# Kernel optimization log

Hardware: AMD Instinct MI355X
Metric: run time of the kernel (lower is better)

Reference implementation:

```python
import jax, jax.numpy as jnp
import numpy as np
import math

N, E = 50000, 800000
N_BASIS, N_ATOM, L = 32, 128, 2
START, STOP = 0.0, 10.0

_idx = [(i, j, L - i - j) for i in range(L + 1) for j in range(L + 1 - i)]
IP = np.array([t[0] for t in _idx], np.float32)
JP = np.array([t[1] for t in _idx], np.float32)
KP = np.array([t[2] for t in _idx], np.float32)
_d = np.array([math.factorial(a) * math.factorial(b) * math.factorial(c) for a, b, c in _idx], np.float32)
PREF2 = np.sqrt(math.factorial(L) / _d).astype(np.float32)  # [T], T = (L+1)(L+2)/2 = 6
OFFSETS = np.linspace(START, STOP, N_BASIS, dtype=np.float32)
WIDTH = np.float32(OFFSETS[1] - OFFSETS[0])


def _signed_pow(x, p):
    # matches torch.pow for negative base with integer-valued float exponent
    p = np.asarray(p)
    odd = (p.astype(np.int64) % 2 == 1)
    r = jnp.abs(x)[:, None] ** jnp.asarray(p)[None, :]
    return jnp.where((x < 0.0)[:, None] & jnp.asarray(odd)[None, :], -r, r)


def setup_inputs() -> dict:
    key = jax.random.key(0)
    ks = jax.random.split(key, 12)
    s = 0.05
    return {
        "feat": jax.random.normal(ks[0], (N, N_ATOM), jnp.float32),
        "dis_vec": jax.random.normal(ks[1], (E, 3), jnp.float32),
        "cj_w1": jax.random.normal(ks[2], (N_ATOM, N_ATOM), jnp.float32) * s,
        "cj_b1": jnp.zeros((N_ATOM,), jnp.float32),
        "cj_w2": jax.random.normal(ks[3], (N_ATOM, 1), jnp.float32) * s,
        "cj_b2": jnp.zeros((1,), jnp.float32),
        "msg_w1": jax.random.normal(ks[4], (N_BASIS, N_ATOM), jnp.float32) * s,
        "msg_b1": jnp.zeros((N_ATOM,), jnp.float32),
        "msg_w2": jax.random.normal(ks[5], (N_ATOM, N_ATOM), jnp.float32) * s,
        "msg_b2": jnp.zeros((N_ATOM,), jnp.float32),
        "filt_w1": jax.random.normal(ks[6], (IP.shape[0], IP.shape[0]), jnp.float32) * s,
        "filt_w2": jax.random.normal(ks[7], (IP.shape[0], 1), jnp.float32) * s,
        "filt_b2": jnp.zeros((1,), jnp.float32),
        "src": jax.random.randint(ks[8], (E,), 0, N, jnp.int32),
        "dst": jax.random.randint(ks[9], (E,), 0, N, jnp.int32),
    }


def reference(feat, dis_vec, cj_w1, cj_b1, cj_w2, cj_b2, msg_w1, msg_b1, msg_w2, msg_b2, filt_w1, filt_w2, filt_b2, src, dst):
    silu = jax.nn.silu  # swish
    # polynomial prefactor: [E, T]
    phix = _signed_pow(dis_vec[:, 0] + 1e-8, IP)
    phiy = _signed_pow(dis_vec[:, 1] + 1e-8, JP)
    phiz = _signed_pow(dis_vec[:, 2] + 1e-8, KP)
    prefactor = phix * phiy * phiz
    # gaussian basis: [E, n_basis] (cutoff_network is None -> C = 1)
    dis = jnp.linalg.norm(dis_vec + 1e-9, axis=-1)
    coeff = -0.5 / (WIDTH ** 2)
    g0 = jnp.exp(coeff * (dis[:, None] - jnp.asarray(OFFSETS)[None, :]) ** 2)
    # gauss: [E, n_basis, T]
    gauss = prefactor[:, None, :] * g0[:, :, None] * jnp.asarray(PREF2)[None, None, :]
    # cj = cj_mlp(feat): [N, 1]
    cj = silu(feat @ cj_w1 + cj_b1) @ cj_w2 + cj_b2
    # e_mul_v: gather dst-node scalar onto edges; copy_e_sum(g.reverse()): scatter-sum to src nodes
    fij = gauss * cj[dst][:, :, None]  # [E, n_basis, T]
    agg = jax.ops.segment_sum(fij, src, num_segments=N)  # [N, n_basis, T]
    f2 = jnp.sum(agg ** 2, axis=-1)  # [N, n_basis]
    msg_in = f2 / (jnp.linalg.norm(f2 + 1e-9, axis=-1, keepdims=True) + 1.0)
    msg_out = silu(msg_in @ msg_w1 + msg_b1) @ msg_w2 + msg_b2  # [N, n_atom_basis]
    gn = gauss / (jnp.linalg.norm(gauss + 1e-8, axis=-1) + 1.0)[..., None]
    filt = (silu(gn @ filt_w1) @ filt_w2 + filt_b2)[..., 0]  # [E, n_basis]
    return msg_out, filt
```

## Files before the change

kernel.cpp:

```cpp
#include <hip/hip_runtime.h>
#include <math.h>

#define N_NODES 50000
#define N_EDGES 800000
#define NB 32
#define NA 128
#define CJ_BLOCKS 782
#define CNT_BLOCKS 3125
#define EDGE_BLOCKS 3125
#define SCAN_BLOCKS 49

constexpr double STEP_D = 10.0 / 31.0;
constexpr float  STEP_F = (float)(10.0 / 31.0);
constexpr float  COEFF  = -0.5f / (STEP_F * STEP_F);
constexpr float  R2     = 1.41421356237309515f;
constexpr float  INV_STEP = 3.1f;
constexpr float  HWIN   = 2.05f;

__device__ __forceinline__ float fast_rcp(float x) {
    return __builtin_amdgcn_rcpf(x);
}

__device__ __forceinline__ float silu_f(float x) {
    return x * fast_rcp(1.0f + __expf(-x));
}

__global__ __launch_bounds__(256) void k_cj_count(const float* __restrict__ feat,
                                                  const float* __restrict__ w1,
                                                  const float* __restrict__ b1,
                                                  const float* __restrict__ w2,
                                                  const float* __restrict__ b2,
                                                  float* __restrict__ cj,
                                                  const int* __restrict__ src,
                                                  int* __restrict__ cnt) {
    __shared__ float fls[64 * 128];
    int tid = threadIdx.x;
    int blk = blockIdx.x;
    if (blk >= CJ_BLOCKS) {
        int e = (blk - CJ_BLOCKS) * 256 + tid;
        if (e < N_EDGES) atomicAdd(&cnt[src[e]], 1);
        return;
    }
    int jq  = tid & 31;
    int ng  = tid >> 5;
    int j0  = jq * 4;
    int n0  = blk * 64;

    {
        const float4* fp = (const float4*)feat;
        int base = n0 * 32;
        int maxi = N_NODES * 32 - 1;
#pragma unroll
        for (int r = 0; r < 8; r++) {
            int idx = base + r * 256 + tid;
            ((float4*)fls)[r * 256 + tid] = fp[min(idx, maxi)];
        }
    }
    __syncthreads();

    float4 bv = *(const float4*)&b1[j0];
    float h[8][4];
#pragma unroll
    for (int i = 0; i < 8; i++) {
        h[i][0] = bv.x; h[i][1] = bv.y; h[i][2] = bv.z; h[i][3] = bv.w;
    }
    for (int kb = 0; kb < 128; kb += 4) {
        float4 wv[4];
#pragma unroll
        for (int u = 0; u < 4; u++) wv[u] = *(const float4*)&w1[(kb + u) * 128 + j0];
#pragma unroll
        for (int i = 0; i < 8; i++) {
            float4 f4 = *(const float4*)&fls[(ng * 8 + i) * 128 + kb];
            h[i][0] = fmaf(f4.x, wv[0].x, h[i][0]);
            h[i][1] = fmaf(f4.x, wv[0].y, h[i][1]);
            h[i][2] = fmaf(f4.x, wv[0].z, h[i][2]);
            h[i][3] = fmaf(f4.x, wv[0].w, h[i][3]);
            h[i][0] = fmaf(f4.y, wv[1].x, h[i][0]);
            h[i][1] = fmaf(f4.y, wv[1].y, h[i][1]);
            h[i][2] = fmaf(f4.y, wv[1].z, h[i][2]);
            h[i][3] = fmaf(f4.y, wv[1].w, h[i][3]);
            h[i][0] = fmaf(f4.z, wv[2].x, h[i][0]);
            h[i][1] = fmaf(f4.z, wv[2].y, h[i][1]);
            h[i][2] = fmaf(f4.z, wv[2].z, h[i][2]);
            h[i][3] = fmaf(f4.z, wv[2].w, h[i][3]);
            h[i][0] = fmaf(f4.w, wv[3].x, h[i][0]);
            h[i][1] = fmaf(f4.w, wv[3].y, h[i][1]);
            h[i][2] = fmaf(f4.w, wv[3].z, h[i][2]);
            h[i][3] = fmaf(f4.w, wv[3].w, h[i][3]);
        }
    }
    float4 w2v = *(const float4*)&w2[j0];
    float keep = 0.f;
#pragma unroll
    for (int i = 0; i < 8; i++) {
        float v = silu_f(h[i][0]) * w2v.x + silu_f(h[i][1]) * w2v.y
                + silu_f(h[i][2]) * w2v.z + silu_f(h[i][3]) * w2v.w;
#pragma unroll
        for (int m = 1; m < 32; m <<= 1) v += __shfl_xor(v, m, 64);
        if (jq == i) keep = v;
    }
    if (jq < 8) {
        int n = n0 + ng * 8 + jq;
        if (n < N_NODES) cj[n] = b2[0] + keep;
    }
}

__global__ __launch_bounds__(1024) void k_scan1(const int* __restrict__ cnt,
                                                int* __restrict__ offs,
                                                int* __restrict__ bsum) {
    __shared__ int s[1024];
    int i = blockIdx.x * 1024 + threadIdx.x;
    int v = (i < N_NODES) ? cnt[i] : 0;
    s[threadIdx.x] = v;
    __syncthreads();
    for (int o = 1; o < 1024; o <<= 1) {
        int t = (threadIdx.x >= (unsigned)o) ? s[threadIdx.x - o] : 0;
        __syncthreads();
        s[threadIdx.x] += t;
        __syncthreads();
    }
    if (i < N_NODES) offs[i] = s[threadIdx.x] - v;
    if (threadIdx.x == 1023) bsum[blockIdx.x] = s[1023];
}

__global__ __launch_bounds__(1024) void k_scan2(int* __restrict__ offs,
                                                const int* __restrict__ bsum,
                                                int* __restrict__ cursor) {
    __shared__ int sbase;
    if (threadIdx.x < 64) {
        int lane = threadIdx.x;
        int v = (lane < blockIdx.x) ? bsum[lane] : 0;
#pragma unroll
        for (int m = 1; m < 64; m <<= 1) v += __shfl_xor(v, m, 64);
        if (lane == 0) sbase = v;
    }
    __syncthreads();
    int i = blockIdx.x * 1024 + threadIdx.x;
    if (i < N_NODES) {
        int v = offs[i] + sbase;
        offs[i] = v;
        cursor[i] = v;
    }
}

__global__ __launch_bounds__(256) void k_edge(const int* __restrict__ src,
                                              const int* __restrict__ dst,
                                              const float* __restrict__ dis_vec,
                                              const float* __restrict__ cj,
                                              int* __restrict__ cursor,
                                              float* __restrict__ sedge,
                                              const float* __restrict__ fw1,
                                              const float* __restrict__ fw2,
                                              const float* __restrict__ fb2,
                                              float* __restrict__ outf) {
    __shared__ float buf[256 * 36];
    int tid = threadIdx.x;
    int e = blockIdx.x * 256 + tid;
    int se = src[e];
    int de = dst[e];
    float dx = dis_vec[3 * e], dy = dis_vec[3 * e + 1], dz = dis_vec[3 * e + 2];
    float cjd = cj[de];
    int p = atomicAdd(&cursor[se], 1);

    float ax = dx + 1e-9f, ay = dy + 1e-9f, az = dz + 1e-9f;
    float dis = sqrtf(ax * ax + ay * ay + az * az);
    float x = dx + 1e-8f, y = dy + 1e-8f, z = dz + 1e-8f;
    float pre[6];
    pre[0] = z * z;      pre[1] = y * z * R2; pre[2] = y * y;
    pre[3] = x * z * R2; pre[4] = x * y * R2; pre[5] = x * x;

    {
        float4* op = (float4*)(sedge + (size_t)p * 8);
        op[0] = make_float4(dis, pre[0] * cjd, pre[1] * cjd, pre[2] * cjd);
        op[1] = make_float4(pre[3] * cjd, pre[4] * cjd, pre[5] * cjd, 0.f);
    }

    float A = 0.f, B = 0.f;
#pragma unroll
    for (int t = 0; t < 6; t++) { A = fmaf(pre[t], pre[t], A); B += pre[t]; }
    float q[6];
#pragma unroll
    for (int tp = 0; tp < 6; tp++) {
        float s = 0.f;
#pragma unroll
        for (int t = 0; t < 6; t++) s = fmaf(pre[t], fw1[t * 6 + tp], s);
        q[tp] = s;
    }
    float bias = fb2[0];
    float w2r[6];
#pragma unroll
    for (int t = 0; t < 6; t++) w2r[t] = fw2[t];

    float* row = &buf[tid * 36];
    float4 b4v = make_float4(bias, bias, bias, bias);
#pragma unroll
    for (int r = 0; r < 8; r++) ((float4*)row)[r] = b4v;

    int b_lo = (int)ceilf((dis - HWIN) * INV_STEP);
#pragma unroll
    for (int k = 0; k < 14; k++) {
        int b = b_lo + k;
        float offb = (float)((double)b * STEP_D);
        float dd = dis - offb;
        float g = __expf(COEFF * dd * dd);
        float ns = fmaf(g * g, A, fmaf(2e-8f * g, B, 6e-16f));
        float rn = fast_rcp(sqrtf(ns) + 1.0f);
        float s = g * rn;
        float o = bias;
#pragma unroll
        for (int tp = 0; tp < 6; tp++) o = fmaf(silu_f(s * q[tp]), w2r[tp], o);
        if ((unsigned)b < 32u) row[b] = o;
    }
    __syncthreads();

    float4* ob = (float4*)(outf + (size_t)blockIdx.x * (256 * 32));
#pragma unroll
    for (int r = 0; r < 8; r++) {
        int g = r * 256 + tid;
        int eloc = g >> 3, j = g & 7;
        ob[g] = *(const float4*)&buf[eloc * 36 + j * 4];
    }
}

__global__ __launch_bounds__(256) void k_agg(const float* __restrict__ sedge,
                                             const int* __restrict__ offs,
                                             const int* __restrict__ cnt,
                                             float* __restrict__ msg_in) {
    int lane = threadIdx.x & 63;
    int n = blockIdx.x * 4 + (threadIdx.x >> 6);
    if (n >= N_NODES) return;
    int b = lane >> 1, th = lane & 1;
    float offb = (float)((double)b * STEP_D);
    int beg = offs[n];
    int deg = cnt[n];
    const float4* sp = (const float4*)sedge + (size_t)beg * 2;
    float a0 = 0.f, a1 = 0.f, a2 = 0.f;
    int i = 0;
    for (; i + 2 <= deg; i += 2) {
        float4 r0 = sp[0], r1 = sp[1], r2 = sp[2], r3 = sp[3];
        sp += 4;
        float dd0 = r0.x - offb;
        float dd1 = r2.x - offb;
        float g0 = __expf(COEFF * dd0 * dd0);
        float g1 = __expf(COEFF * dd1 * dd1);
        float w00 = th ? r1.x : r0.y, w01 = th ? r1.y : r0.z, w02 = th ? r1.z : r0.w;
        float w10 = th ? r3.x : r2.y, w11 = th ? r3.y : r2.z, w12 = th ? r3.z : r2.w;
        a0 = fmaf(g0, w00, a0);
        a1 = fmaf(g0, w01, a1);
        a2 = fmaf(g0, w02, a2);
        a0 = fmaf(g1, w10, a0);
        a1 = fmaf(g1, w11, a1);
        a2 = fmaf(g1, w12, a2);
    }
    if (i < deg) {
        float4 r0 = sp[0], r1 = sp[1];
        float dd0 = r0.x - offb;
        float g0 = __expf(COEFF * dd0 * dd0);
        float w00 = th ? r1.x : r0.y, w01 = th ? r1.y : r0.z, w02 = th ? r1.z : r0.w;
        a0 = fmaf(g0, w00, a0);
        a1 = fmaf(g0, w01, a1);
        a2 = fmaf(g0, w02, a2);
    }
    float s = a0 * a0 + a1 * a1 + a2 * a2;
    float f2 = s + __shfl_xor(s, 1, 64);
    float p = f2 + 1e-9f;
    p = p * p;
    float tot = p;
#pragma unroll
    for (int m = 1; m < 64; m <<= 1) tot += __shfl_xor(tot, m, 64);
    float nrm = sqrtf(0.5f * tot);
    float val = f2 * fast_rcp(nrm + 1.0f);
    if (th == 0) msg_in[(size_t)n * NB + b] = val;
}

__global__ __launch_bounds__(256) void k_msg(const float* __restrict__ msg_in,
                                             const float* __restrict__ w1,
                                             const float* __restrict__ b1,
                                             const float* __restrict__ w2,
                                             const float* __restrict__ b2,
                                             float* __restrict__ out) {
    __shared__ float mi[64 * 32];
    __shared__ float sh[64 * 128];
    int tid = threadIdx.x;
    int jq  = tid & 31;
    int ng  = tid >> 5;
    int j0  = jq * 4;
    int n0  = blockIdx.x * 64;

    {
        const float4* srcp = (const float4*)msg_in;
        int base = n0 * 8;
        int maxi = N_NODES * 8 - 1;
#pragma unroll
        for (int r = 0; r < 2; r++) {
            int idx = base + r * 256 + tid;
            ((float4*)mi)[r * 256 + tid] = srcp[min(idx, maxi)];
        }
    }
    __syncthreads();

    float4 b1v = *(const float4*)&b1[j0];
    float h[8][4];
#pragma unroll
    for (int i = 0; i < 8; i++) {
        h[i][0] = b1v.x; h[i][1] = b1v.y; h[i][2] = b1v.z; h[i][3] = b1v.w;
    }
#pragma unroll
    for (int bb = 0; bb < 32; bb += 4) {
        float4 wv[4];
#pragma unroll
        for (int u = 0; u < 4; u++) wv[u] = *(const float4*)&w1[(bb + u) * 128 + j0];
#pragma unroll
        for (int i = 0; i < 8; i++) {
            float4 m4 = *(const float4*)&mi[(ng * 8 + i) * 32 + bb];
            h[i][0] = fmaf(m4.x, wv[0].x, h[i][0]);
            h[i][1] = fmaf(m4.x, wv[0].y, h[i][1]);
            h[i][2] = fmaf(m4.x, wv[0].z, h[i][2]);
            h[i][3] = fmaf(m4.x, wv[0].w, h[i][3]);
            h[i][0] = fmaf(m4.y, wv[1].x, h[i][0]);
            h[i][1] = fmaf(m4.y, wv[1].y, h[i][1]);
            h[i][2] = fmaf(m4.y, wv[1].z, h[i][2]);
            h[i][3] = fmaf(m4.y, wv[1].w, h[i][3]);
            h[i][0] = fmaf(m4.z, wv[2].x, h[i][0]);
            h[i][1] = fmaf(m4.z, wv[2].y, h[i][1]);
            h[i][2] = fmaf(m4.z, wv[2].z, h[i][2]);
            h[i][3] = fmaf(m4.z, wv[2].w, h[i][3]);
            h[i][0] = fmaf(m4.w, wv[3].x, h[i][0]);
            h[i][1] = fmaf(m4.w, wv[3].y, h[i][1]);
            h[i][2] = fmaf(m4.w, wv[3].z, h[i][2]);
            h[i][3] = fmaf(m4.w, wv[3].w, h[i][3]);
        }
    }
#pragma unroll
    for (int i = 0; i < 8; i++) {
        float4 sv = make_float4(silu_f(h[i][0]), silu_f(h[i][1]),
                                silu_f(h[i][2]), silu_f(h[i][3]));
        *(float4*)&sh[(ng * 8 + i) * 128 + j0] = sv;
    }
    __syncthreads();

    float4 b2v = *(const float4*)&b2[j0];
    float acc[8][4];
#pragma unroll
    for (int i = 0; i < 8; i++) {
        acc[i][0] = b2v.x; acc[i][1] = b2v.y; acc[i][2] = b2v.z; acc[i][3] = b2v.w;
    }
    for (int hb = 0; hb < 128; hb += 4) {
        float4 wv[4];
#pragma unroll
        for (int u = 0; u < 4; u++) wv[u] = *(const float4*)&w2[(hb + u) * 128 + j0];
#pragma unroll
        for (int i = 0; i < 8; i++) {
            float4 s4 = *(const float4*)&sh[(ng * 8 + i) * 128 + hb];
            acc[i][0] = fmaf(s4.x, wv[0].x, acc[i][0]);
            acc[i][1] = fmaf(s4.x, wv[0].y, acc[i][1]);
            acc[i][2] = fmaf(s4.x, wv[0].z, acc[i][2]);
            acc[i][3] = fmaf(s4.x, wv[0].w, acc[i][3]);
            acc[i][0] = fmaf(s4.y, wv[1].x, acc[i][0]);
            acc[i][1] = fmaf(s4.y, wv[1].y, acc[i][1]);
            acc[i][2] = fmaf(s4.y, wv[1].z, acc[i][2]);
            acc[i][3] = fmaf(s4.y, wv[1].w, acc[i][3]);
            acc[i][0] = fmaf(s4.z, wv[2].x, acc[i][0]);
            acc[i][1] = fmaf(s4.z, wv[2].y, acc[i][1]);
            acc[i][2] = fmaf(s4.z, wv[2].z, acc[i][2]);
            acc[i][3] = fmaf(s4.z, wv[2].w, acc[i][3]);
            acc[i][0] = fmaf(s4.w, wv[3].x, acc[i][0]);
            acc[i][1] = fmaf(s4.w, wv[3].y, acc[i][1]);
            acc[i][2] = fmaf(s4.w, wv[3].z, acc[i][2]);
            acc[i][3] = fmaf(s4.w, wv[3].w, acc[i][3]);
        }
    }
#pragma unroll
    for (int i = 0; i < 8; i++) {
        int n = n0 + ng * 8 + i;
        if (n < N_NODES) {
            *(float4*)&out[(size_t)n * 128 + j0] =
                make_float4(acc[i][0], acc[i][1], acc[i][2], acc[i][3]);
        }
    }
}

extern "C" void kernel_launch(void* const* d_in, const int* in_sizes, int n_in,
                              void* d_out, int out_size, void* d_ws, size_t ws_size,
                              hipStream_t stream) {
    (void)in_sizes; (void)n_in; (void)out_size; (void)ws_size;
    const float* feat    = (const float*)d_in[0];
    const float* dis_vec = (const float*)d_in[1];
    const float* cj_w1   = (const float*)d_in[2];
    const float* cj_b1   = (const float*)d_in[3];
    const float* cj_w2   = (const float*)d_in[4];
    const float* cj_b2   = (const float*)d_in[5];
    const float* msg_w1  = (const float*)d_in[6];
    const float* msg_b1  = (const float*)d_in[7];
    const float* msg_w2  = (const float*)d_in[8];
    const float* msg_b2  = (const float*)d_in[9];
    const float* filt_w1 = (const float*)d_in[10];
    const float* filt_w2 = (const float*)d_in[11];
    const float* filt_b2 = (const float*)d_in[12];
    const int*   src     = (const int*)d_in[13];
    const int*   dst     = (const int*)d_in[14];
    float* out = (float*)d_out;

    float* ws     = (float*)d_ws;
    float* cj     = ws;
    float* msg_in = cj + 50048;
    int*   cnt    = (int*)(msg_in + 1600256);
    int*   offs   = cnt + 50048;
    int*   cursor = offs + 50048;
    int*   bsum   = cursor + 50048;
    int*   bbase  = bsum + 64;
    float* sedge  = (float*)(bbase + 64);

    hipMemsetAsync(cnt, 0, N_NODES * sizeof(int), stream);

    k_cj_count<<<CJ_BLOCKS + CNT_BLOCKS, 256, 0, stream>>>(feat, cj_w1, cj_b1, cj_w2,
                                                           cj_b2, cj, src, cnt);
    k_scan1<<<SCAN_BLOCKS, 1024, 0, stream>>>(cnt, offs, bsum);
    k_scan2<<<SCAN_BLOCKS, 1024, 0, stream>>>(offs, bsum, cursor);
    k_edge<<<EDGE_BLOCKS, 256, 0, stream>>>(src, dst, dis_vec, cj, cursor, sedge,
                                            filt_w1, filt_w2, filt_b2,
                                            out + (size_t)N_NODES * NA);
    k_agg<<<(N_NODES + 3) / 4, 256, 0, stream>>>(sedge, offs, cnt, msg_in);
    k_msg<<<(N_NODES + 63) / 64, 256, 0, stream>>>(msg_in, msg_w1, msg_b1, msg_w2, msg_b2, out);
}
```

Before: 350.4 us.

## Fuse scan passes with decoupled lookback and merge aggregation into message MLP

The two scan kernels become one kernel that publishes block sums through atomics and spin-waits on earlier blocks (a decoupled-lookback style prefix). The per-node aggregation kernel is folded into the message MLP kernel. Each wave aggregates 16 nodes into shared memory, which removes the msg_in round trip through global memory and two launches. The cost is fewer blocks and wave-serial per-node loops with shuffle-heavy inner work, which lowers aggregation parallelism. The spin-wait also relies on all 49 scan blocks being co-resident.

```diff
diff --git a/kernel.cpp b/kernel.cpp
--- a/kernel.cpp
+++ b/kernel.cpp
@@ -9,6 +9,7 @@
 #define CNT_BLOCKS 3125
 #define EDGE_BLOCKS 3125
 #define SCAN_BLOCKS 49
+#define AGG_BLOCKS 782
 
 constexpr double STEP_D = 10.0 / 31.0;
 constexpr float  STEP_F = (float)(10.0 / 31.0);
@@ -105,11 +106,14 @@
     }
 }
 
-__global__ __launch_bounds__(1024) void k_scan1(const int* __restrict__ cnt,
-                                                int* __restrict__ offs,
-                                                int* __restrict__ bsum) {
+__global__ __launch_bounds__(1024) void k_scan(const int* __restrict__ cnt,
+                                               int* __restrict__ offs,
+                                               int* __restrict__ cursor,
+                                               int* __restrict__ bsum) {
     __shared__ int s[1024];
-    int i = blockIdx.x * 1024 + threadIdx.x;
+    __shared__ int sbase;
+    int bid = blockIdx.x;
+    int i = bid * 1024 + threadIdx.x;
     int v = (i < N_NODES) ? cnt[i] : 0;
     s[threadIdx.x] = v;
     __syncthreads();
@@ -119,27 +123,24 @@
         s[threadIdx.x] += t;
         __syncthreads();
     }
-    if (i < N_NODES) offs[i] = s[threadIdx.x] - v;
-    if (threadIdx.x == 1023) bsum[blockIdx.x] = s[1023];
-}
-
-__global__ __launch_bounds__(1024) void k_scan2(int* __restrict__ offs,
-                                                const int* __restrict__ bsum,
-                                                int* __restrict__ cursor) {
-    __shared__ int sbase;
+    if (threadIdx.x == 1023) atomicExch(&bsum[bid], s[1023] + 1);
     if (threadIdx.x < 64) {
         int lane = threadIdx.x;
-        int v = (lane < blockIdx.x) ? bsum[lane] : 0;
-#pragma unroll
-        for (int m = 1; m < 64; m <<= 1) v += __shfl_xor(v, m, 64);
-        if (lane == 0) sbase = v;
-    }
-    __syncthreads();
-    int i = blockIdx.x * 1024 + threadIdx.x;
+        int val = 0;
+        if (lane < bid) {
+            int t;
+            do { t = atomicAdd(&bsum[lane], 0); } while (t == 0);
+            val = t - 1;
+        }
+#pragma unroll
+        for (int m = 1; m < 64; m <<= 1) val += __shfl_xor(val, m, 64);
+        if (lane == 0) sbase = val;
+    }
+    __syncthreads();
     if (i < N_NODES) {
-        int v = offs[i] + sbase;
-        offs[i] = v;
-        cursor[i] = v;
+        int o2 = s[threadIdx.x] - v + sbase;
+        offs[i] = o2;
+        cursor[i] = o2;
     }
 }
 
@@ -222,82 +223,68 @@
     }
 }
 
-__global__ __launch_bounds__(256) void k_agg(const float* __restrict__ sedge,
-                                             const int* __restrict__ offs,
-                                             const int* __restrict__ cnt,
-                                             float* __restrict__ msg_in) {
-    int lane = threadIdx.x & 63;
-    int n = blockIdx.x * 4 + (threadIdx.x >> 6);
-    if (n >= N_NODES) return;
-    int b = lane >> 1, th = lane & 1;
-    float offb = (float)((double)b * STEP_D);
-    int beg = offs[n];
-    int deg = cnt[n];
-    const float4* sp = (const float4*)sedge + (size_t)beg * 2;
-    float a0 = 0.f, a1 = 0.f, a2 = 0.f;
-    int i = 0;
-    for (; i + 2 <= deg; i += 2) {
-        float4 r0 = sp[0], r1 = sp[1], r2 = sp[2], r3 = sp[3];
-        sp += 4;
-        float dd0 = r0.x - offb;
-        float dd1 = r2.x - offb;
-        float g0 = __expf(COEFF * dd0 * dd0);
-        float g1 = __expf(COEFF * dd1 * dd1);
-        float w00 = th ? r1.x : r0.y, w01 = th ? r1.y : r0.z, w02 = th ? r1.z : r0.w;
-        float w10 = th ? r3.x : r2.y, w11 = th ? r3.y : r2.z, w12 = th ? r3.z : r2.w;
-        a0 = fmaf(g0, w00, a0);
-        a1 = fmaf(g0, w01, a1);
-        a2 = fmaf(g0, w02, a2);
-        a0 = fmaf(g1, w10, a0);
-        a1 = fmaf(g1, w11, a1);
-        a2 = fmaf(g1, w12, a2);
-    }
-    if (i < deg) {
-        float4 r0 = sp[0], r1 = sp[1];
-        float dd0 = r0.x - offb;
-        float g0 = __expf(COEFF * dd0 * dd0);
-        float w00 = th ? r1.x : r0.y, w01 = th ? r1.y : r0.z, w02 = th ? r1.z : r0.w;
-        a0 = fmaf(g0, w00, a0);
-        a1 = fmaf(g0, w01, a1);
-        a2 = fmaf(g0, w02, a2);
-    }
-    float s = a0 * a0 + a1 * a1 + a2 * a2;
-    float f2 = s + __shfl_xor(s, 1, 64);
-    float p = f2 + 1e-9f;
-    p = p * p;
-    float tot = p;
-#pragma unroll
-    for (int m = 1; m < 64; m <<= 1) tot += __shfl_xor(tot, m, 64);
-    float nrm = sqrtf(0.5f * tot);
-    float val = f2 * fast_rcp(nrm + 1.0f);
-    if (th == 0) msg_in[(size_t)n * NB + b] = val;
-}
-
-__global__ __launch_bounds__(256) void k_msg(const float* __restrict__ msg_in,
-                                             const float* __restrict__ w1,
-                                             const float* __restrict__ b1,
-                                             const float* __restrict__ w2,
-                                             const float* __restrict__ b2,
-                                             float* __restrict__ out) {
+__global__ __launch_bounds__(256) void k_aggmsg(const float* __restrict__ sedge,
+                                                const int* __restrict__ offs,
+                                                const int* __restrict__ cnt,
+                                                const float* __restrict__ w1,
+                                                const float* __restrict__ b1,
+                                                const float* __restrict__ w2,
+                                                const float* __restrict__ b2,
+                                                float* __restrict__ out) {
     __shared__ float mi[64 * 32];
     __shared__ float sh[64 * 128];
     int tid = threadIdx.x;
+    int wv = tid >> 6, lane = tid & 63;
+    int n0 = blockIdx.x * 64;
+    int b = lane >> 1, th = lane & 1;
+    float offb = (float)((double)b * STEP_D);
+    const float4* sp4 = (const float4*)sedge;
+
+    int pn = n0 + wv * 16 + (lane & 15);
+    int pbeg = 0, pdeg = 0;
+    if (pn < N_NODES) { pbeg = offs[pn]; pdeg = cnt[pn]; }
+
+    for (int u = 0; u < 16; u++) {
+        int beg = __shfl(pbeg, u, 64);
+        int deg = __shfl(pdeg, u, 64);
+        float a0 = 0.f, a1 = 0.f, a2 = 0.f;
+        for (int c0 = 0; c0 < deg; c0 += 32) {
+            int rem = deg - c0;
+            int m = rem < 32 ? rem : 32;
+            int li = lane < 2 * m ? lane : 2 * m - 1;
+            float4 r = sp4[(size_t)(beg + c0) * 2 + li];
+            float v0 = (lane & 1) ? r.x : r.y;
+            float v1 = (lane & 1) ? r.y : r.z;
+            float v2 = (lane & 1) ? r.z : r.w;
+            for (int e2 = 0; e2 < m; e2++) {
+                int sl = 2 * e2;
+                float dis = __shfl(r.x, sl, 64);
+                float w0 = __shfl(v0, sl + th, 64);
+                float w1v = __shfl(v1, sl + th, 64);
+                float w2v = __shfl(v2, sl + th, 64);
+                float dd = dis - offb;
+                float g = __expf(COEFF * dd * dd);
+                a0 = fmaf(g, w0, a0);
+                a1 = fmaf(g, w1v, a1);
+                a2 = fmaf(g, w2v, a2);
+            }
+        }
+        float s2 = a0 * a0 + a1 * a1 + a2 * a2;
+        float f2 = s2 + __shfl_xor(s2, 1, 64);
+        float p = f2 + 1e-9f;
+        p = p * p;
+        float tot = p;
+#pragma unroll
+        for (int mm = 1; mm < 64; mm <<= 1) tot += __shfl_xor(tot, mm, 64);
+        float nrm = sqrtf(0.5f * tot);
+        float val = f2 * fast_rcp(nrm + 1.0f);
+        if (th == 0) mi[(wv * 16 + u) * 32 + b] = val;
+    }
+    __syncthreads();
+
     int jq  = tid & 31;
     int ng  = tid >> 5;
     int j0  = jq * 4;
-    int n0  = blockIdx.x * 64;
-
-    {
-        const float4* srcp = (const float4*)msg_in;
-        int base = n0 * 8;
-        int maxi = N_NODES * 8 - 1;
-#pragma unroll
-        for (int r = 0; r < 2; r++) {
-            int idx = base + r * 256 + tid;
-            ((float4*)mi)[r * 256 + tid] = srcp[min(idx, maxi)];
-        }
-    }
-    __syncthreads();
 
     float4 b1v = *(const float4*)&b1[j0];
     float h[8][4];
@@ -307,28 +294,28 @@
     }
 #pragma unroll
     for (int bb = 0; bb < 32; bb += 4) {
-        float4 wv[4];
-#pragma unroll
-        for (int u = 0; u < 4; u++) wv[u] = *(const float4*)&w1[(bb + u) * 128 + j0];
+        float4 wvv[4];
+#pragma unroll
+        for (int u = 0; u < 4; u++) wvv[u] = *(const float4*)&w1[(bb + u) * 128 + j0];
 #pragma unroll
         for (int i = 0; i < 8; i++) {
             float4 m4 = *(const float4*)&mi[(ng * 8 + i) * 32 + bb];
-            h[i][0] = fmaf(m4.x, wv[0].x, h[i][0]);
-            h[i][1] = fmaf(m4.x, wv[0].y, h[i][1]);
-            h[i][2] = fmaf(m4.x, wv[0].z, h[i][2]);
-            h[i][3] = fmaf(m4.x, wv[0].w, h[i][3]);
-            h[i][0] = fmaf(m4.y, wv[1].x, h[i][0]);
-            h[i][1] = fmaf(m4.y, wv[1].y, h[i][1]);
-            h[i][2] = fmaf(m4.y, wv[1].z, h[i][2]);
-            h[i][3] = fmaf(m4.y, wv[1].w, h[i][3]);
-            h[i][0] = fmaf(m4.z, wv[2].x, h[i][0]);
-            h[i][1] = fmaf(m4.z, wv[2].y, h[i][1]);
-            h[i][2] = fmaf(m4.z, wv[2].z, h[i][2]);
-            h[i][3] = fmaf(m4.z, wv[2].w, h[i][3]);
-            h[i][0] = fmaf(m4.w, wv[3].x, h[i][0]);
-            h[i][1] = fmaf(m4.w, wv[3].y, h[i][1]);
-            h[i][2] = fmaf(m4.w, wv[3].z, h[i][2]);
-            h[i][3] = fmaf(m4.w, wv[3].w, h[i][3]);
+            h[i][0] = fmaf(m4.x, wvv[0].x, h[i][0]);
+            h[i][1] = fmaf(m4.x, wvv[0].y, h[i][1]);
+            h[i][2] = fmaf(m4.x, wvv[0].z, h[i][2]);
+            h[i][3] = fmaf(m4.x, wvv[0].w, h[i][3]);
+            h[i][0] = fmaf(m4.y, wvv[1].x, h[i][0]);
+            h[i][1] = fmaf(m4.y, wvv[1].y, h[i][1]);
+            h[i][2] = fmaf(m4.y, wvv[1].z, h[i][2]);
+            h[i][3] = fmaf(m4.y, wvv[1].w, h[i][3]);
+            h[i][0] = fmaf(m4.z, wvv[2].x, h[i][0]);
+            h[i][1] = fmaf(m4.z, wvv[2].y, h[i][1]);
+            h[i][2] = fmaf(m4.z, wvv[2].z, h[i][2]);
+            h[i][3] = fmaf(m4.z, wvv[2].w, h[i][3]);
+            h[i][0] = fmaf(m4.w, wvv[3].x, h[i][0]);
+            h[i][1] = fmaf(m4.w, wvv[3].y, h[i][1]);
+            h[i][2] = fmaf(m4.w, wvv[3].z, h[i][2]);
+            h[i][3] = fmaf(m4.w, wvv[3].w, h[i][3]);
         }
     }
 #pragma unroll
@@ -346,28 +333,28 @@
         acc[i][0] = b2v.x; acc[i][1] = b2v.y; acc[i][2] = b2v.z; acc[i][3] = b2v.w;
     }
     for (int hb = 0; hb < 128; hb += 4) {
-        float4 wv[4];
-#pragma unroll
-        for (int u = 0; u < 4; u++) wv[u] = *(const float4*)&w2[(hb + u) * 128 + j0];
+        float4 wvv[4];
+#pragma unroll
+        for (int u = 0; u < 4; u++) wvv[u] = *(const float4*)&w2[(hb + u) * 128 + j0];
 #pragma unroll
         for (int i = 0; i < 8; i++) {
             float4 s4 = *(const float4*)&sh[(ng * 8 + i) * 128 + hb];
-            acc[i][0] = fmaf(s4.x, wv[0].x, acc[i][0]);
-            acc[i][1] = fmaf(s4.x, wv[0].y, acc[i][1]);
-            acc[i][2] = fmaf(s4.x, wv[0].z, acc[i][2]);
-            acc[i][3] = fmaf(s4.x, wv[0].w, acc[i][3]);
-            acc[i][0] = fmaf(s4.y, wv[1].x, acc[i][0]);
-            acc[i][1] = fmaf(s4.y, wv[1].y, acc[i][1]);
-            acc[i][2] = fmaf(s4.y, wv[1].z, acc[i][2]);
-            acc[i][3] = fmaf(s4.y, wv[1].w, acc[i][3]);
-            acc[i][0] = fmaf(s4.z, wv[2].x, acc[i][0]);
-            acc[i][1] = fmaf(s4.z, wv[2].y, acc[i][1]);
-            acc[i][2] = fmaf(s4.z, wv[2].z, acc[i][2]);
-            acc[i][3] = fmaf(s4.z, wv[2].w, acc[i][3]);
-            acc[i][0] = fmaf(s4.w, wv[3].x, acc[i][0]);
-            acc[i][1] = fmaf(s4.w, wv[3].y, acc[i][1]);
-            acc[i][2] = fmaf(s4.w, wv[3].z, acc[i][2]);
-            acc[i][3] = fmaf(s4.w, wv[3].w, acc[i][3]);
+            acc[i][0] = fmaf(s4.x, wvv[0].x, acc[i][0]);
+            acc[i][1] = fmaf(s4.x, wvv[0].y, acc[i][1]);
+            acc[i][2] = fmaf(s4.x, wvv[0].z, acc[i][2]);
+            acc[i][3] = fmaf(s4.x, wvv[0].w, acc[i][3]);
+            acc[i][0] = fmaf(s4.y, wvv[1].x, acc[i][0]);
+            acc[i][1] = fmaf(s4.y, wvv[1].y, acc[i][1]);
+            acc[i][2] = fmaf(s4.y, wvv[1].z, acc[i][2]);
+            acc[i][3] = fmaf(s4.y, wvv[1].w, acc[i][3]);
+            acc[i][0] = fmaf(s4.z, wvv[2].x, acc[i][0]);
+            acc[i][1] = fmaf(s4.z, wvv[2].y, acc[i][1]);
+            acc[i][2] = fmaf(s4.z, wvv[2].z, acc[i][2]);
+            acc[i][3] = fmaf(s4.z, wvv[2].w, acc[i][3]);
+            acc[i][0] = fmaf(s4.w, wvv[3].x, acc[i][0]);
+            acc[i][1] = fmaf(s4.w, wvv[3].y, acc[i][1]);
+            acc[i][2] = fmaf(s4.w, wvv[3].z, acc[i][2]);
+            acc[i][3] = fmaf(s4.w, wvv[3].w, acc[i][3]);
         }
     }
 #pragma unroll
@@ -403,23 +390,20 @@
 
     float* ws     = (float*)d_ws;
     float* cj     = ws;
-    float* msg_in = cj + 50048;
-    int*   cnt    = (int*)(msg_in + 1600256);
-    int*   offs   = cnt + 50048;
+    int*   cnt    = (int*)(cj + 50048);
+    int*   bsum   = cnt + 50048;
+    int*   offs   = bsum + 64;
     int*   cursor = offs + 50048;
-    int*   bsum   = cursor + 50048;
-    int*   bbase  = bsum + 64;
-    float* sedge  = (float*)(bbase + 64);
-
-    hipMemsetAsync(cnt, 0, N_NODES * sizeof(int), stream);
+    float* sedge  = (float*)(cursor + 50048);
+
+    hipMemsetAsync(cnt, 0, (50048 + 64) * sizeof(int), stream);
 
     k_cj_count<<<CJ_BLOCKS + CNT_BLOCKS, 256, 0, stream>>>(feat, cj_w1, cj_b1, cj_w2,
                                                            cj_b2, cj, src, cnt);
-    k_scan1<<<SCAN_BLOCKS, 1024, 0, stream>>>(cnt, offs, bsum);
-    k_scan2<<<SCAN_BLOCKS, 1024, 0, stream>>>(offs, bsum, cursor);
+    k_scan<<<SCAN_BLOCKS, 1024, 0, stream>>>(cnt, offs, cursor, bsum);
     k_edge<<<EDGE_BLOCKS, 256, 0, stream>>>(src, dst, dis_vec, cj, cursor, sedge,
                                             filt_w1, filt_w2, filt_b2,
                                             out + (size_t)N_NODES * NA);
-    k_agg<<<(N_NODES + 3) / 4, 256, 0, stream>>>(sedge, offs, cnt, msg_in);
-    k_msg<<<(N_NODES + 63) / 64, 256, 0, stream>>>(msg_in, msg_w1, msg_b1, msg_w2, msg_b2, out);
-}
+    k_aggmsg<<<AGG_BLOCKS, 256, 0, stream>>>(sedge, offs, cnt,
+                                             msg_w1, msg_b1, msg_w2, msg_b2, out);
+}
```

Result: slower. 368.5 us (+5.2%).

## Merge two-pass scan into single-pass spin-wait scan and unroll agg loads

Applied to the files above, without the earlier changes.

Replaces the two scan kernels with one kernel where each block publishes its total (offset by one so zero means not ready) and spins on earlier blocks' totals with atomics, removing one launch and the reread of offs. The workspace is reordered so bsum sits right after cnt and is cleared by the same memset. The aggregation loop now loads 8 edges (16 float4) at once before computing, to raise memory-level parallelism. The spin-wait relies on all 49 blocks being co-resident, and the larger unroll raises register use.

```diff
diff --git a/kernel.cpp b/kernel.cpp
--- a/kernel.cpp
+++ b/kernel.cpp
@@ -105,11 +105,14 @@
     }
 }
 
-__global__ __launch_bounds__(1024) void k_scan1(const int* __restrict__ cnt,
-                                                int* __restrict__ offs,
-                                                int* __restrict__ bsum) {
+__global__ __launch_bounds__(1024) void k_scan(const int* __restrict__ cnt,
+                                               int* __restrict__ offs,
+                                               int* __restrict__ cursor,
+                                               int* __restrict__ bsum) {
     __shared__ int s[1024];
-    int i = blockIdx.x * 1024 + threadIdx.x;
+    __shared__ int sbase;
+    int bid = blockIdx.x;
+    int i = bid * 1024 + threadIdx.x;
     int v = (i < N_NODES) ? cnt[i] : 0;
     s[threadIdx.x] = v;
     __syncthreads();
@@ -119,27 +122,24 @@
         s[threadIdx.x] += t;
         __syncthreads();
     }
-    if (i < N_NODES) offs[i] = s[threadIdx.x] - v;
-    if (threadIdx.x == 1023) bsum[blockIdx.x] = s[1023];
-}
-
-__global__ __launch_bounds__(1024) void k_scan2(int* __restrict__ offs,
-                                                const int* __restrict__ bsum,
-                                                int* __restrict__ cursor) {
-    __shared__ int sbase;
+    if (threadIdx.x == 1023) atomicExch(&bsum[bid], s[1023] + 1);
     if (threadIdx.x < 64) {
         int lane = threadIdx.x;
-        int v = (lane < blockIdx.x) ? bsum[lane] : 0;
-#pragma unroll
-        for (int m = 1; m < 64; m <<= 1) v += __shfl_xor(v, m, 64);
-        if (lane == 0) sbase = v;
-    }
-    __syncthreads();
-    int i = blockIdx.x * 1024 + threadIdx.x;
+        int val = 0;
+        if (lane < bid) {
+            int t;
+            do { t = atomicAdd(&bsum[lane], 0); } while (t == 0);
+            val = t - 1;
+        }
+#pragma unroll
+        for (int m = 1; m < 64; m <<= 1) val += __shfl_xor(val, m, 64);
+        if (lane == 0) sbase = val;
+    }
+    __syncthreads();
     if (i < N_NODES) {
-        int v = offs[i] + sbase;
-        offs[i] = v;
-        cursor[i] = v;
+        int o2 = s[threadIdx.x] - v + sbase;
+        offs[i] = o2;
+        cursor[i] = o2;
     }
 }
 
@@ -236,30 +236,35 @@
     const float4* sp = (const float4*)sedge + (size_t)beg * 2;
     float a0 = 0.f, a1 = 0.f, a2 = 0.f;
     int i = 0;
-    for (; i + 2 <= deg; i += 2) {
-        float4 r0 = sp[0], r1 = sp[1], r2 = sp[2], r3 = sp[3];
-        sp += 4;
-        float dd0 = r0.x - offb;
-        float dd1 = r2.x - offb;
-        float g0 = __expf(COEFF * dd0 * dd0);
-        float g1 = __expf(COEFF * dd1 * dd1);
-        float w00 = th ? r1.x : r0.y, w01 = th ? r1.y : r0.z, w02 = th ? r1.z : r0.w;
-        float w10 = th ? r3.x : r2.y, w11 = th ? r3.y : r2.z, w12 = th ? r3.z : r2.w;
-        a0 = fmaf(g0, w00, a0);
-        a1 = fmaf(g0, w01, a1);
-        a2 = fmaf(g0, w02, a2);
-        a0 = fmaf(g1, w10, a0);
-        a1 = fmaf(g1, w11, a1);
-        a2 = fmaf(g1, w12, a2);
-    }
-    if (i < deg) {
+    for (; i + 8 <= deg; i += 8) {
+        float4 r[16];
+#pragma unroll
+        for (int u = 0; u < 16; u++) r[u] = sp[u];
+        sp += 16;
+#pragma unroll
+        for (int u = 0; u < 8; u++) {
+            float4 r0 = r[2 * u], r1 = r[2 * u + 1];
+            float dd = r0.x - offb;
+            float g = __expf(COEFF * dd * dd);
+            float w0 = th ? r1.x : r0.y;
+            float w1 = th ? r1.y : r0.z;
+            float w2 = th ? r1.z : r0.w;
+            a0 = fmaf(g, w0, a0);
+            a1 = fmaf(g, w1, a1);
+            a2 = fmaf(g, w2, a2);
+        }
+    }
+    for (; i < deg; i++) {
         float4 r0 = sp[0], r1 = sp[1];
-        float dd0 = r0.x - offb;
-        float g0 = __expf(COEFF * dd0 * dd0);
-        float w00 = th ? r1.x : r0.y, w01 = th ? r1.y : r0.z, w02 = th ? r1.z : r0.w;
-        a0 = fmaf(g0, w00, a0);
-        a1 = fmaf(g0, w01, a1);
-        a2 = fmaf(g0, w02, a2);
+        sp += 2;
+        float dd = r0.x - offb;
+        float g = __expf(COEFF * dd * dd);
+        float w0 = th ? r1.x : r0.y;
+        float w1 = th ? r1.y : r0.z;
+        float w2 = th ? r1.z : r0.w;
+        a0 = fmaf(g, w0, a0);
+        a1 = fmaf(g, w1, a1);
+        a2 = fmaf(g, w2, a2);
     }
     float s = a0 * a0 + a1 * a1 + a2 * a2;
     float f2 = s + __shfl_xor(s, 1, 64);
@@ -403,20 +408,18 @@
 
     float* ws     = (float*)d_ws;
     float* cj     = ws;
-    float* msg_in = cj + 50048;
-    int*   cnt    = (int*)(msg_in + 1600256);
-    int*   offs   = cnt + 50048;
+    int*   cnt    = (int*)(cj + 50048);
+    int*   bsum   = cnt + 50048;
+    int*   offs   = bsum + 64;
     int*   cursor = offs + 50048;
-    int*   bsum   = cursor + 50048;
-    int*   bbase  = bsum + 64;
-    float* sedge  = (float*)(bbase + 64);
-
-    hipMemsetAsync(cnt, 0, N_NODES * sizeof(int), stream);
+    float* msg_in = (float*)(cursor + 50048);
+    float* sedge  = msg_in + 1600256;
+
+    hipMemsetAsync(cnt, 0, (50048 + 64) * sizeof(int), stream);
 
     k_cj_count<<<CJ_BLOCKS + CNT_BLOCKS, 256, 0, stream>>>(feat, cj_w1, cj_b1, cj_w2,
                                                            cj_b2, cj, src, cnt);
-    k_scan1<<<SCAN_BLOCKS, 1024, 0, stream>>>(cnt, offs, bsum);
-    k_scan2<<<SCAN_BLOCKS, 1024, 0, stream>>>(offs, bsum, cursor);
+    k_scan<<<SCAN_BLOCKS, 1024, 0, stream>>>(cnt, offs, cursor, bsum);
     k_edge<<<EDGE_BLOCKS, 256, 0, stream>>>(src, dst, dis_vec, cj, cursor, sedge,
                                             filt_w1, filt_w2, filt_b2,
                                             out + (size_t)N_NODES * NA);
```

After: 350.6 us. No clear change (+0.1%).
